# Kernel tuning notes

Measured on AMD Instinct MI355X. Metric: run time of the kernel, lower is better.

## Reference

```python
import jax, jax.numpy as jnp
import numpy as np
from jax import lax

IN_CH = 256
OUT_CH = 256
INTER = IN_CH // 2
KERNEL = 3


def setup_inputs() -> dict:
    key = jax.random.key(0)
    ks = jax.random.split(key, 6)
    B, C, H, W = 8, IN_CH, 128, 128
    x = jax.random.normal(ks[0], (B, C, H, W), dtype=jnp.float32)
    s = 1.0 / np.sqrt(C)
    Wq = jax.random.normal(ks[1], (INTER, C), dtype=jnp.float32) * s
    Wk = jax.random.normal(ks[2], (INTER, C), dtype=jnp.float32) * s
    Wv = jax.random.normal(ks[3], (INTER, C), dtype=jnp.float32) * s
    w1d = jax.random.normal(ks[4], (KERNEL,), dtype=jnp.float32) * (1.0 / np.sqrt(KERNEL))
    Wc = jax.random.normal(ks[5], (OUT_CH, INTER, 3, 3), dtype=jnp.float32) * (1.0 / np.sqrt(INTER * 9))
    return {"x": x, "Wq": Wq, "Wk": Wk, "Wv": Wv, "w1d": w1d, "Wc": Wc}


def reference(x, Wq, Wk, Wv, w1d, Wc):
    B, C, H, W = x.shape
    inter = Wq.shape[0]
    Hs, Ws = H // 4, W // 4  # 1x1 conv, stride 4, pad 0 == spatial subsample
    xs = x[:, :, ::4, ::4]  # [B, C, Hs, Ws]
    q = jnp.einsum('oc,bchw->bohw', Wq, xs).reshape(B, inter, Hs * Ws)  # [B, inter, N]
    k = jnp.einsum('oc,bchw->bohw', Wk, xs).reshape(B, inter, Hs * Ws)
    v = jnp.einsum('oc,bchw->bohw', Wv, xs).reshape(B, inter, Hs * Ws)
    # gate = softmax(Q^T K) over last dim, shape [B, N, N]
    scores = jnp.einsum('bcn,bcm->bnm', q, k)
    gate = jax.nn.softmax(scores, axis=-1)
    # gated value: [B, inter, N] -> [B, inter, Hs, Ws]
    gv = jnp.einsum('bnm,bcm->bcn', gate, v).reshape(B, inter, Hs, Ws)
    # ECA channel gating: global avg pool -> conv1d over channel dim -> sigmoid
    ca = gv.mean(axis=(2, 3))  # [B, inter]
    ca = lax.conv_general_dilated(
        ca[:, None, :],                     # [B, 1, inter]
        w1d[None, None, :],                 # [1, 1, K]
        window_strides=(1,), padding=[((KERNEL - 1) // 2,) * 2],
        dimension_numbers=('NCH', 'OIH', 'NCH'))
    ca = jax.nn.sigmoid(ca)[:, 0, :, None, None]  # [B, inter, 1, 1]
    out = gv * ca
    out = lax.conv_general_dilated(
        out, Wc, window_strides=(1, 1), padding='SAME',
        dimension_numbers=('NCHW', 'OIHW', 'NCHW'))
    return out, gate, ca
```

## Files before the change

### kernel.cpp

```cpp
#include <hip/hip_runtime.h>
#include <math.h>

#define B_   8
#define C_   256
#define CI_  128
#define N_   1024
#define HW_  32
#define CO_  256

typedef __bf16 v8bf __attribute__((ext_vector_type(8)));
typedef float  f32x4 __attribute__((ext_vector_type(4)));
typedef unsigned short ushort_t;

__device__ __forceinline__ unsigned short f2bf_rne(float f) {
    unsigned int u = __float_as_uint(f);
    unsigned int r = u + 0x7FFF + ((u >> 16) & 1);
    return (unsigned short)(r >> 16);
}
__device__ __forceinline__ float bf2f(unsigned short h) {
    return __uint_as_float(((unsigned int)h) << 16);
}
__device__ __forceinline__ v8bf ld8(const ushort_t* p) {
    return *(const v8bf*)p;
}

__global__ __launch_bounds__(256) void prep_all_kernel(
    const float* __restrict__ x,
    const float* __restrict__ Wc,
    const float* __restrict__ Wq, const float* __restrict__ Wk,
    const float* __restrict__ Wv,
    ushort_t* __restrict__ Whi, ushort_t* __restrict__ Wlo,
    ushort_t* __restrict__ Wp_hi, ushort_t* __restrict__ Wp_lo,
    ushort_t* __restrict__ xs_hi, ushort_t* __restrict__ xs_lo,
    float* __restrict__ meanb)
{
    __shared__ ushort_t lh[32 * 264];
    __shared__ ushort_t ll[32 * 264];
    const int bx = blockIdx.x;
    const int tid = threadIdx.x;

    if (bx < 1152) {
        if (bx == 0) {
            *(float4*)&meanb[tid * 4] = make_float4(0.f, 0.f, 0.f, 0.f);
        }
        int idx = bx * 256 + tid;
        int o = idx / 1152;
        int r = idx - o * 1152;
        int ci = r / 9;
        int tap = r - ci * 9;
        float v = Wc[idx];
        unsigned short h = f2bf_rne(v);
        unsigned short l = f2bf_rne(v - bf2f(h));
        int didx = o * 1152 + tap * 128 + ci;
        Whi[didx] = h; Wlo[didx] = l;
    } else if (bx < 1536) {
        int j = (bx - 1152) * 256 + tid;
        int o = j >> 8, c = j & 255;
        float v = (o < 128) ? Wq[o * 256 + c]
                : (o < 256) ? Wk[(o - 128) * 256 + c]
                            : Wv[(o - 256) * 256 + c];
        unsigned short h = f2bf_rne(v);
        unsigned short l = f2bf_rne(v - bf2f(h));
        Wp_hi[j] = h; Wp_lo[j] = l;
    } else {
        const int bx2 = bx - 1536;
        const int h = bx2 & 31, b = bx2 >> 5;
        const int w = tid & 31, cg = tid >> 5;
        float v[32];
        #pragma unroll
        for (int i = 0; i < 32; ++i) {
            int c = i * 8 + cg;
            v[i] = x[((size_t)(b * C_ + c) * 128 + h * 4) * 128 + w * 4];
        }
        #pragma unroll
        for (int i = 0; i < 32; ++i) {
            int c = i * 8 + cg;
            unsigned short hi = f2bf_rne(v[i]);
            unsigned short lo = f2bf_rne(v[i] - bf2f(hi));
            lh[w * 264 + c] = hi;
            ll[w * 264 + c] = lo;
        }
        __syncthreads();
        const int ww = tid >> 3, cs = tid & 7;
        size_t dst = ((size_t)(b * N_) + h * 32 + ww) * 256 + cs * 32;
        #pragma unroll
        for (int t = 0; t < 4; ++t) {
            *(uint4*)&xs_hi[dst + t * 8] = *(uint4*)&lh[ww * 264 + cs * 32 + t * 8];
            *(uint4*)&xs_lo[dst + t * 8] = *(uint4*)&ll[ww * 264 + cs * 32 + t * 8];
        }
    }
}

__global__ __launch_bounds__(256) void proj_mfma_kernel(
    const ushort_t* __restrict__ Wp_hi, const ushort_t* __restrict__ Wp_lo,
    const ushort_t* __restrict__ xs_hi, const ushort_t* __restrict__ xs_lo,
    ushort_t* __restrict__ qt_hi, ushort_t* __restrict__ qt_lo,
    ushort_t* __restrict__ kt_hi, ushort_t* __restrict__ kt_lo,
    ushort_t* __restrict__ vB_hi, ushort_t* __restrict__ vB_lo)
{
    const int n0 = blockIdx.x * 64;
    const int o0 = blockIdx.y * 64;
    const int b  = blockIdx.z;
    const int tid = threadIdx.x;
    const int l = tid & 63, wv = tid >> 6;
    const int wy = wv >> 1, wx = wv & 1;
    const int ln = l & 15, quad = l >> 4;

    f32x4 acc[2][2];
    #pragma unroll
    for (int i = 0; i < 2; ++i)
        #pragma unroll
        for (int j = 0; j < 2; ++j) acc[i][j] = (f32x4){0.f,0.f,0.f,0.f};

    const ushort_t* Ah_p[2]; const ushort_t* Al_p[2];
    const ushort_t* Bh_p[2]; const ushort_t* Bl_p[2];
    #pragma unroll
    for (int i = 0; i < 2; ++i) {
        size_t off = (size_t)(o0 + wy * 32 + i * 16 + ln) * 256 + quad * 8;
        Ah_p[i] = Wp_hi + off; Al_p[i] = Wp_lo + off;
    }
    #pragma unroll
    for (int j = 0; j < 2; ++j) {
        size_t off = ((size_t)(b * N_) + n0 + wx * 32 + j * 16 + ln) * 256 + quad * 8;
        Bh_p[j] = xs_hi + off; Bl_p[j] = xs_lo + off;
    }

    #pragma unroll 4
    for (int k0 = 0; k0 < 256; k0 += 32) {
        v8bf Ah[2], Al[2], Bh[2], Bl[2];
        #pragma unroll
        for (int i = 0; i < 2; ++i) { Ah[i] = ld8(Ah_p[i] + k0); Al[i] = ld8(Al_p[i] + k0); }
        #pragma unroll
        for (int j = 0; j < 2; ++j) { Bh[j] = ld8(Bh_p[j] + k0); Bl[j] = ld8(Bl_p[j] + k0); }
        #pragma unroll
        for (int i = 0; i < 2; ++i)
            #pragma unroll
            for (int j = 0; j < 2; ++j) {
                acc[i][j] = __builtin_amdgcn_mfma_f32_16x16x32_bf16(Ah[i], Bh[j], acc[i][j], 0, 0, 0);
                acc[i][j] = __builtin_amdgcn_mfma_f32_16x16x32_bf16(Ah[i], Bl[j], acc[i][j], 0, 0, 0);
                acc[i][j] = __builtin_amdgcn_mfma_f32_16x16x32_bf16(Al[i], Bh[j], acc[i][j], 0, 0, 0);
            }
    }

    if (o0 < 256) {
        ushort_t* th = (o0 < 128) ? qt_hi : kt_hi;
        ushort_t* tl = (o0 < 128) ? qt_lo : kt_lo;
        const int ob = o0 & 127;
        #pragma unroll
        for (int i = 0; i < 2; ++i)
            #pragma unroll
            for (int j = 0; j < 2; ++j) {
                int oo = ob + wy * 32 + i * 16 + quad * 4;
                int n  = n0 + wx * 32 + j * 16 + ln;
                unsigned int h01 = 0, h23 = 0, l01 = 0, l23 = 0;
                #pragma unroll
                for (int r = 0; r < 4; ++r) {
                    float f = acc[i][j][r];
                    unsigned short hh = f2bf_rne(f);
                    unsigned short lo = f2bf_rne(f - bf2f(hh));
                    if (r < 2) { h01 |= ((unsigned)hh) << (16 * r); l01 |= ((unsigned)lo) << (16 * r); }
                    else       { h23 |= ((unsigned)hh) << (16 * (r - 2)); l23 |= ((unsigned)lo) << (16 * (r - 2)); }
                }
                size_t off = ((size_t)(b * N_) + n) * 128 + oo;
                *(uint2*)&th[off] = make_uint2(h01, h23);
                *(uint2*)&tl[off] = make_uint2(l01, l23);
            }
    } else {
        #pragma unroll
        for (int i = 0; i < 2; ++i)
            #pragma unroll
            for (int j = 0; j < 2; ++j)
                #pragma unroll
                for (int r = 0; r < 4; ++r) {
                    int c = (o0 - 256) + wy * 32 + i * 16 + quad * 4 + r;
                    int m = n0 + wx * 32 + j * 16 + ln;
                    float f = acc[i][j][r];
                    unsigned short hh = f2bf_rne(f);
                    unsigned short lo = f2bf_rne(f - bf2f(hh));
                    size_t off = (((size_t)b * 32 + (m >> 5)) * 128 + c) * 32 + (m & 31);
                    vB_hi[off] = hh; vB_lo[off] = lo;
                }
    }
}

__global__ __launch_bounds__(512, 2) void attn_fused_kernel(
    const ushort_t* __restrict__ qt_hi, const ushort_t* __restrict__ qt_lo,
    const ushort_t* __restrict__ kt_hi, const ushort_t* __restrict__ kt_lo,
    const ushort_t* __restrict__ vB_hi, const ushort_t* __restrict__ vB_lo,
    float* __restrict__ gate, float* __restrict__ gv, float* __restrict__ meanb)
{
    __shared__ __align__(16) char gsm[65536];
    __shared__ float redA[8][32];
    __shared__ float redB[8][32];

    const int n0 = blockIdx.x * 32;
    const int b  = blockIdx.y;
    const int tid = threadIdx.x;
    const int l = tid & 63, w = tid >> 6;
    const int ln = l & 15, quad = l >> 4;
    const int Mw = w * 128;

    const ushort_t* qb_h = qt_hi + ((size_t)(b * N_) + n0) * 128;
    const ushort_t* qb_l = qt_lo + ((size_t)(b * N_) + n0) * 128;
    const ushort_t* kb_h = kt_hi + (size_t)(b * N_) * 128;
    const ushort_t* kb_l = kt_lo + (size_t)(b * N_) * 128;

    f32x4 acc[2][8];
    #pragma unroll
    for (int nt = 0; nt < 2; ++nt)
        #pragma unroll
        for (int mt = 0; mt < 8; ++mt) acc[nt][mt] = (f32x4){0.f,0.f,0.f,0.f};

    #pragma unroll
    for (int c0 = 0; c0 < 128; c0 += 32) {
        v8bf Ah[2], Al[2];
        #pragma unroll
        for (int nt = 0; nt < 2; ++nt) {
            size_t aoff = (size_t)(nt * 16 + ln) * 128 + c0 + quad * 8;
            Ah[nt] = ld8(qb_h + aoff); Al[nt] = ld8(qb_l + aoff);
        }
        #pragma unroll
        for (int mt = 0; mt < 8; ++mt) {
            size_t boff = (size_t)(Mw + mt * 16 + ln) * 128 + c0 + quad * 8;
            v8bf Bh = ld8(kb_h + boff);
            v8bf Bl = ld8(kb_l + boff);
            #pragma unroll
            for (int nt = 0; nt < 2; ++nt) {
                acc[nt][mt] = __builtin_amdgcn_mfma_f32_16x16x32_bf16(Ah[nt], Bh, acc[nt][mt], 0, 0, 0);
                acc[nt][mt] = __builtin_amdgcn_mfma_f32_16x16x32_bf16(Ah[nt], Bl, acc[nt][mt], 0, 0, 0);
                acc[nt][mt] = __builtin_amdgcn_mfma_f32_16x16x32_bf16(Al[nt], Bh, acc[nt][mt], 0, 0, 0);
            }
        }
    }

    float rmax[2][4];
    #pragma unroll
    for (int nt = 0; nt < 2; ++nt)
        #pragma unroll
        for (int r = 0; r < 4; ++r) {
            float m = acc[nt][0][r];
            #pragma unroll
            for (int mt = 1; mt < 8; ++mt) m = fmaxf(m, acc[nt][mt][r]);
            rmax[nt][r] = m;
        }
    #pragma unroll
    for (int nt = 0; nt < 2; ++nt)
        #pragma unroll
        for (int r = 0; r < 4; ++r) {
            float m = rmax[nt][r];
            #pragma unroll
            for (int xm = 1; xm <= 8; xm <<= 1) m = fmaxf(m, __shfl_xor(m, xm, 64));
            rmax[nt][r] = m;
        }
    if (ln == 0) {
        #pragma unroll
        for (int nt = 0; nt < 2; ++nt)
            #pragma unroll
            for (int r = 0; r < 4; ++r)
                redA[w][nt * 16 + quad * 4 + r] = rmax[nt][r];
    }
    __syncthreads();
    #pragma unroll
    for (int nt = 0; nt < 2; ++nt)
        #pragma unroll
        for (int r = 0; r < 4; ++r) {
            int row = nt * 16 + quad * 4 + r;
            float m0 = fmaxf(fmaxf(redA[0][row], redA[1][row]),
                             fmaxf(redA[2][row], redA[3][row]));
            float m1 = fmaxf(fmaxf(redA[4][row], redA[5][row]),
                             fmaxf(redA[6][row], redA[7][row]));
            rmax[nt][r] = fmaxf(m0, m1);
        }

    float rsum[2][4];
    #pragma unroll
    for (int nt = 0; nt < 2; ++nt)
        #pragma unroll
        for (int r = 0; r < 4; ++r) {
            float s = 0.f;
            #pragma unroll
            for (int mt = 0; mt < 8; ++mt) {
                float e = __expf(acc[nt][mt][r] - rmax[nt][r]);
                acc[nt][mt][r] = e;
                s += e;
            }
            rsum[nt][r] = s;
        }
    #pragma unroll
    for (int nt = 0; nt < 2; ++nt)
        #pragma unroll
        for (int r = 0; r < 4; ++r) {
            float s = rsum[nt][r];
            #pragma unroll
            for (int xm = 1; xm <= 8; xm <<= 1) s += __shfl_xor(s, xm, 64);
            rsum[nt][r] = s;
        }
    if (ln == 0) {
        #pragma unroll
        for (int nt = 0; nt < 2; ++nt)
            #pragma unroll
            for (int r = 0; r < 4; ++r)
                redB[w][nt * 16 + quad * 4 + r] = rsum[nt][r];
    }
    __syncthreads();
    #pragma unroll
    for (int nt = 0; nt < 2; ++nt)
        #pragma unroll
        for (int r = 0; r < 4; ++r) {
            int row = nt * 16 + quad * 4 + r;
            float inv = 1.0f / ((redB[0][row] + redB[1][row] + redB[2][row] + redB[3][row]) +
                                (redB[4][row] + redB[5][row] + redB[6][row] + redB[7][row]));
            #pragma unroll
            for (int mt = 0; mt < 8; ++mt) acc[nt][mt][r] *= inv;
        }

    float* grow = gate + (size_t)b * N_ * N_;
    #pragma unroll
    for (int nt = 0; nt < 2; ++nt)
        #pragma unroll
        for (int r = 0; r < 4; ++r) {
            int n  = n0 + nt * 16 + quad * 4 + r;
            int nl = nt * 16 + quad * 4 + r;
            #pragma unroll
            for (int mt = 0; mt < 8; ++mt) {
                int m = Mw + mt * 16 + ln;
                float v = acc[nt][mt][r];
                grow[(size_t)n * N_ + m] = v;
                int chunk = m >> 3;
                int addr = nl * 2048 + (((chunk ^ (nl & 7))) << 4) + ((m & 7) << 1);
                *(ushort_t*)&gsm[addr] = f2bf_rne(v);
            }
        }
    __syncthreads();

    const ushort_t* vb_h = vB_hi + (size_t)b * CI_ * N_;
    const ushort_t* vb_l = vB_lo + (size_t)b * CI_ * N_;

    f32x4 acc2[2];
    acc2[0] = (f32x4){0.f,0.f,0.f,0.f};
    acc2[1] = (f32x4){0.f,0.f,0.f,0.f};

    #pragma unroll 4
    for (int m0 = 0; m0 < 1024; m0 += 32) {
        v8bf Bg[2];
        #pragma unroll
        for (int nt = 0; nt < 2; ++nt) {
            int nl = nt * 16 + ln;
            int chunk = (m0 >> 3) + quad;
            Bg[nt] = *(const v8bf*)&gsm[nl * 2048 + (((chunk ^ (nl & 7))) << 4)];
        }
        int c = w * 16 + ln;
        size_t aoff = (((size_t)(m0 >> 5)) * 128 + c) * 32 + quad * 8;
        v8bf Avh = ld8(vb_h + aoff);
        v8bf Avl = ld8(vb_l + aoff);
        #pragma unroll
        for (int nt = 0; nt < 2; ++nt) {
            acc2[nt] = __builtin_amdgcn_mfma_f32_16x16x32_bf16(Avh, Bg[nt], acc2[nt], 0, 0, 0);
            acc2[nt] = __builtin_amdgcn_mfma_f32_16x16x32_bf16(Avl, Bg[nt], acc2[nt], 0, 0, 0);
        }
    }

    #pragma unroll
    for (int nt = 0; nt < 2; ++nt) {
        int n = n0 + nt * 16 + ln;
        float4 o4 = make_float4(acc2[nt][0], acc2[nt][1], acc2[nt][2], acc2[nt][3]);
        *(float4*)&gv[((size_t)(b * N_) + n) * CI_ + w * 16 + quad * 4] = o4;
    }

    float s0 = acc2[0][0] + acc2[1][0];
    float s1 = acc2[0][1] + acc2[1][1];
    float s2 = acc2[0][2] + acc2[1][2];
    float s3 = acc2[0][3] + acc2[1][3];
    #pragma unroll
    for (int xm = 1; xm <= 8; xm <<= 1) {
        s0 += __shfl_xor(s0, xm, 64);
        s1 += __shfl_xor(s1, xm, 64);
        s2 += __shfl_xor(s2, xm, 64);
        s3 += __shfl_xor(s3, xm, 64);
    }
    if (ln == 0) {
        int cb = b * CI_ + w * 16 + quad * 4;
        atomicAdd(&meanb[cb + 0], s0);
        atomicAdd(&meanb[cb + 1], s1);
        atomicAdd(&meanb[cb + 2], s2);
        atomicAdd(&meanb[cb + 3], s3);
    }
}

__global__ __launch_bounds__(1024) void ca_kernel(
    const float* __restrict__ meanb, const float* __restrict__ w1d,
    float* __restrict__ ca)
{
    const int t = threadIdx.x;
    const int i = t & 127;
    const float sc = 1.0f / 1024.0f;
    float left  = (i > 0)   ? meanb[t - 1] * sc : 0.0f;
    float mid   = meanb[t] * sc;
    float right = (i < 127) ? meanb[t + 1] * sc : 0.0f;
    float val = w1d[0] * left + w1d[1] * mid + w1d[2] * right;
    ca[t] = 1.0f / (1.0f + __expf(-val));
}

#define BHI  0
#define BLO  17408
__global__ __launch_bounds__(256) void conv_mfma_kernel(
    const float* __restrict__ gv, const float* __restrict__ ca,
    const ushort_t* __restrict__ Whi, const ushort_t* __restrict__ Wlo,
    float* __restrict__ out)
{
    __shared__ __align__(16) char smem[67584];
    const int AH[2] = {34816, 51200};
    const int AL[2] = {43008, 59392};

    const int b   = blockIdx.z;
    const int h0  = blockIdx.y * 2;
    const int o0  = blockIdx.x * 64;
    const int tid = threadIdx.x;
    const int l   = tid & 63;
    const int wv  = tid >> 6;
    const int wy  = wv >> 1;
    const int wx  = wv & 1;
    const int ln  = l & 15;
    const int quad = l >> 4;

    f32x4 acc[2][2];
    #pragma unroll
    for (int i = 0; i < 2; ++i)
        #pragma unroll
        for (int j = 0; j < 2; ++j)
            acc[i][j] = (f32x4){0.f, 0.f, 0.f, 0.f};

    const int srow0 = tid >> 3, scol = tid & 7;
    const int la0 = srow0 * 128 + scol * 16;
    const int la1 = (srow0 + 32) * 128 + scol * 16;

    for (int half = 0; half < 2; ++half) {
        __syncthreads();
        for (int u = tid; u < 136 * 16; u += 256) {
            int p   = u >> 4;
            int ciq = u & 15;
            int hrel = p / 34;
            int c    = p - hrel * 34;
            int gr = h0 + hrel - 1;
            int gc = c - 1;
            bool ok = ((unsigned)gr < 32u) && ((unsigned)gc < 32u);
            int cib = half * 64 + ciq * 4;
            float vv[4] = {0.f, 0.f, 0.f, 0.f};
            if (ok) {
                float4 v4 = *(const float4*)&gv[((size_t)(b * N_) + gr * 32 + gc) * CI_ + cib];
                float4 c4 = *(const float4*)&ca[b * CI_ + cib];
                vv[0] = v4.x * c4.x; vv[1] = v4.y * c4.y;
                vv[2] = v4.z * c4.z; vv[3] = v4.w * c4.w;
            }
            unsigned int hx = 0, hy = 0, lx = 0, ly = 0;
            #pragma unroll
            for (int t = 0; t < 4; ++t) {
                unsigned short h = f2bf_rne(vv[t]);
                unsigned short lo = f2bf_rne(vv[t] - bf2f(h));
                if (t < 2) { hx |= ((unsigned)h) << (16 * t); lx |= ((unsigned)lo) << (16 * t); }
                else       { hy |= ((unsigned)h) << (16 * (t - 2)); ly |= ((unsigned)lo) << (16 * (t - 2)); }
            }
            int addr = p * 128 + (((ciq >> 1) ^ (p & 7)) << 4) + ((ciq & 1) << 3);
            *(uint2*)&smem[BHI + addr] = make_uint2(hx, hy);
            *(uint2*)&smem[BLO + addr] = make_uint2(lx, ly);
        }
        {
            int csrc0 = scol ^ (srow0 & 7);
            int csrc1 = scol ^ ((srow0 + 32) & 7);
            size_t g0 = (size_t)(o0 + srow0) * 1152 + half * 64 + csrc0 * 8;
            size_t g1 = (size_t)(o0 + srow0 + 32) * 1152 + half * 64 + csrc1 * 8;
            uint4 h0r = *(const uint4*)&Whi[g0];
            uint4 l0r = *(const uint4*)&Wlo[g0];
            uint4 h1r = *(const uint4*)&Whi[g1];
            uint4 l1r = *(const uint4*)&Wlo[g1];
            *(uint4*)&smem[AH[0] + la0] = h0r;
            *(uint4*)&smem[AL[0] + la0] = l0r;
            *(uint4*)&smem[AH[0] + la1] = h1r;
            *(uint4*)&smem[AL[0] + la1] = l1r;
        }

        for (int tap = 0; tap < 9; ++tap) {
            __syncthreads();
            uint4 nh0, nl0, nh1, nl1;
            if (tap < 8) {
                int ntap = tap + 1;
                int csrc0 = scol ^ (srow0 & 7);
                int csrc1 = scol ^ ((srow0 + 32) & 7);
                size_t g0 = (size_t)(o0 + srow0) * 1152 + ntap * 128 + half * 64 + csrc0 * 8;
                size_t g1 = (size_t)(o0 + srow0 + 32) * 1152 + ntap * 128 + half * 64 + csrc1 * 8;
                nh0 = *(const uint4*)&Whi[g0];
                nl0 = *(const uint4*)&Wlo[g0];
                nh1 = *(const uint4*)&Whi[g1];
                nl1 = *(const uint4*)&Wlo[g1];
            }
            const int ah = AH[tap & 1], al = AL[tap & 1];
            const int dy = tap / 3, dx = tap - dy * 3;
            const int pbase = (wx + dy) * 34 + dx;
            #pragma unroll
            for (int cc = 0; cc < 2; ++cc) {
                v8bf Bh[2], Bl[2], Ah2[2], Al2[2];
                #pragma unroll
                for (int j = 0; j < 2; ++j) {
                    int p = pbase + j * 16 + ln;
                    int ch = cc * 4 + quad;
                    int addr = p * 128 + ((ch ^ (p & 7)) << 4);
                    Bh[j] = *(const v8bf*)&smem[BHI + addr];
                    Bl[j] = *(const v8bf*)&smem[BLO + addr];
                }
                #pragma unroll
                for (int i = 0; i < 2; ++i) {
                    int o = wy * 32 + i * 16 + ln;
                    int ch = cc * 4 + quad;
                    int addr = o * 128 + ((ch ^ (o & 7)) << 4);
                    Ah2[i] = *(const v8bf*)&smem[ah + addr];
                    Al2[i] = *(const v8bf*)&smem[al + addr];
                }
                #pragma unroll
                for (int i = 0; i < 2; ++i)
                    #pragma unroll
                    for (int j = 0; j < 2; ++j) {
                        acc[i][j] = __builtin_amdgcn_mfma_f32_16x16x32_bf16(Ah2[i], Bh[j], acc[i][j], 0, 0, 0);
                        acc[i][j] = __builtin_amdgcn_mfma_f32_16x16x32_bf16(Ah2[i], Bl[j], acc[i][j], 0, 0, 0);
                        acc[i][j] = __builtin_amdgcn_mfma_f32_16x16x32_bf16(Al2[i], Bh[j], acc[i][j], 0, 0, 0);
                    }
            }
            if (tap < 8) {
                int nb = (tap + 1) & 1;
                *(uint4*)&smem[AH[nb] + la0] = nh0;
                *(uint4*)&smem[AL[nb] + la0] = nl0;
                *(uint4*)&smem[AH[nb] + la1] = nh1;
                *(uint4*)&smem[AL[nb] + la1] = nl1;
            }
        }
    }

    const int h = h0 + wx;
    #pragma unroll
    for (int i = 0; i < 2; ++i)
        #pragma unroll
        for (int j = 0; j < 2; ++j)
            #pragma unroll
            for (int r = 0; r < 4; ++r) {
                int o = o0 + wy * 32 + i * 16 + quad * 4 + r;
                int w = j * 16 + ln;
                out[(size_t)(b * CO_ + o) * N_ + h * 32 + w] = acc[i][j][r];
            }
}

extern "C" void kernel_launch(void* const* d_in, const int* in_sizes, int n_in,
                              void* d_out, int out_size, void* d_ws, size_t ws_size,
                              hipStream_t stream) {
    const float* x   = (const float*)d_in[0];
    const float* Wq  = (const float*)d_in[1];
    const float* Wk  = (const float*)d_in[2];
    const float* Wv  = (const float*)d_in[3];
    const float* w1d = (const float*)d_in[4];
    const float* Wc  = (const float*)d_in[5];

    float* out  = (float*)d_out;
    float* gate = out + 2097152;
    float* ca   = gate + 8388608;

    float*    gv      = (float*)d_ws;
    float*    meanb   = gv + 1048576;
    ushort_t* Whi     = (ushort_t*)(meanb + 1024);
    ushort_t* Wlo     = Whi + 294912;
    ushort_t* Wp_hi   = Wlo + 294912;
    ushort_t* Wp_lo   = Wp_hi + 98304;
    ushort_t* xs_hi   = Wp_lo + 98304;
    ushort_t* xs_lo   = xs_hi + 2097152;
    ushort_t* qt_hi   = xs_lo + 2097152;
    ushort_t* qt_lo   = qt_hi + 1048576;
    ushort_t* kt_hi   = qt_lo + 1048576;
    ushort_t* kt_lo   = kt_hi + 1048576;
    ushort_t* vB_hi   = kt_lo + 1048576;
    ushort_t* vB_lo   = vB_hi + 1048576;

    prep_all_kernel<<<dim3(1792), 256, 0, stream>>>(
        x, Wc, Wq, Wk, Wv, Whi, Wlo, Wp_hi, Wp_lo, xs_hi, xs_lo, meanb);
    proj_mfma_kernel<<<dim3(16, 6, 8), 256, 0, stream>>>(
        Wp_hi, Wp_lo, xs_hi, xs_lo, qt_hi, qt_lo, kt_hi, kt_lo, vB_hi, vB_lo);
    attn_fused_kernel<<<dim3(32, 8), 512, 0, stream>>>(
        qt_hi, qt_lo, kt_hi, kt_lo, vB_hi, vB_lo, gate, gv, meanb);
    ca_kernel<<<1, 1024, 0, stream>>>(meanb, w1d, ca);
    conv_mfma_kernel<<<dim3(4, 16, 8), 256, 0, stream>>>(gv, ca, Whi, Wlo, out);
}
```

Measured before the change: 286.8 us.

## Fuse ECA gate into conv, remap block order, add MFMA priority, defer gate store

The separate ca_kernel launch is removed: each conv block now computes the 128 sigmoid channel gates from meanb into shared memory, and one block per batch writes ca out. Block indices in the projection, attention and conv kernels are remapped so the batch index varies fastest, spreading work across XCDs and caches. s_setprio wraps the MFMA bursts to favour matrix issue over other waves. The fp32 gate store in the attention kernel moves after the gv MFMA loop so the large global write overlaps less with the compute phase. In exchange, every conv block repeats the small gate computation.

Result: no change. 284.0 us (-1.0%).

```diff
diff --git a/kernel.cpp b/kernel.cpp
--- a/kernel.cpp
+++ b/kernel.cpp
@@ -98,9 +98,11 @@
     ushort_t* __restrict__ kt_hi, ushort_t* __restrict__ kt_lo,
     ushort_t* __restrict__ vB_hi, ushort_t* __restrict__ vB_lo)
 {
-    const int n0 = blockIdx.x * 64;
-    const int o0 = blockIdx.y * 64;
-    const int b  = blockIdx.z;
+    const int lin = blockIdx.x + 16 * (blockIdx.y + 6 * blockIdx.z);
+    const int b    = lin & 7;
+    const int rest = lin >> 3;
+    const int n0 = (rest & 15) * 64;
+    const int o0 = (rest >> 4) * 64;
     const int tid = threadIdx.x;
     const int l = tid & 63, wv = tid >> 6;
     const int wy = wv >> 1, wx = wv & 1;
@@ -132,6 +134,7 @@
         for (int i = 0; i < 2; ++i) { Ah[i] = ld8(Ah_p[i] + k0); Al[i] = ld8(Al_p[i] + k0); }
         #pragma unroll
         for (int j = 0; j < 2; ++j) { Bh[j] = ld8(Bh_p[j] + k0); Bl[j] = ld8(Bl_p[j] + k0); }
+        __builtin_amdgcn_s_setprio(1);
         #pragma unroll
         for (int i = 0; i < 2; ++i)
             #pragma unroll
@@ -140,6 +143,7 @@
                 acc[i][j] = __builtin_amdgcn_mfma_f32_16x16x32_bf16(Ah[i], Bl[j], acc[i][j], 0, 0, 0);
                 acc[i][j] = __builtin_amdgcn_mfma_f32_16x16x32_bf16(Al[i], Bh[j], acc[i][j], 0, 0, 0);
             }
+        __builtin_amdgcn_s_setprio(0);
     }
 
     if (o0 < 256) {
@@ -193,8 +197,9 @@
     __shared__ float redA[8][32];
     __shared__ float redB[8][32];
 
-    const int n0 = blockIdx.x * 32;
-    const int b  = blockIdx.y;
+    const int lin = blockIdx.x + 32 * blockIdx.y;
+    const int b  = lin & 7;
+    const int n0 = (lin >> 3) * 32;
     const int tid = threadIdx.x;
     const int l = tid & 63, w = tid >> 6;
     const int ln = l & 15, quad = l >> 4;
@@ -224,12 +229,14 @@
             size_t boff = (size_t)(Mw + mt * 16 + ln) * 128 + c0 + quad * 8;
             v8bf Bh = ld8(kb_h + boff);
             v8bf Bl = ld8(kb_l + boff);
+            __builtin_amdgcn_s_setprio(1);
             #pragma unroll
             for (int nt = 0; nt < 2; ++nt) {
                 acc[nt][mt] = __builtin_amdgcn_mfma_f32_16x16x32_bf16(Ah[nt], Bh, acc[nt][mt], 0, 0, 0);
                 acc[nt][mt] = __builtin_amdgcn_mfma_f32_16x16x32_bf16(Ah[nt], Bl, acc[nt][mt], 0, 0, 0);
                 acc[nt][mt] = __builtin_amdgcn_mfma_f32_16x16x32_bf16(Al[nt], Bh, acc[nt][mt], 0, 0, 0);
             }
+            __builtin_amdgcn_s_setprio(0);
         }
     }
 
@@ -314,21 +321,17 @@
             for (int mt = 0; mt < 8; ++mt) acc[nt][mt][r] *= inv;
         }
 
-    float* grow = gate + (size_t)b * N_ * N_;
-    #pragma unroll
-    for (int nt = 0; nt < 2; ++nt)
-        #pragma unroll
-        for (int r = 0; r < 4; ++r) {
-            int n  = n0 + nt * 16 + quad * 4 + r;
+    #pragma unroll
+    for (int nt = 0; nt < 2; ++nt)
+        #pragma unroll
+        for (int r = 0; r < 4; ++r) {
             int nl = nt * 16 + quad * 4 + r;
             #pragma unroll
             for (int mt = 0; mt < 8; ++mt) {
                 int m = Mw + mt * 16 + ln;
-                float v = acc[nt][mt][r];
-                grow[(size_t)n * N_ + m] = v;
                 int chunk = m >> 3;
                 int addr = nl * 2048 + (((chunk ^ (nl & 7))) << 4) + ((m & 7) << 1);
-                *(ushort_t*)&gsm[addr] = f2bf_rne(v);
+                *(ushort_t*)&gsm[addr] = f2bf_rne(acc[nt][mt][r]);
             }
         }
     __syncthreads();
@@ -353,11 +356,13 @@
         size_t aoff = (((size_t)(m0 >> 5)) * 128 + c) * 32 + quad * 8;
         v8bf Avh = ld8(vb_h + aoff);
         v8bf Avl = ld8(vb_l + aoff);
+        __builtin_amdgcn_s_setprio(1);
         #pragma unroll
         for (int nt = 0; nt < 2; ++nt) {
             acc2[nt] = __builtin_amdgcn_mfma_f32_16x16x32_bf16(Avh, Bg[nt], acc2[nt], 0, 0, 0);
             acc2[nt] = __builtin_amdgcn_mfma_f32_16x16x32_bf16(Avl, Bg[nt], acc2[nt], 0, 0, 0);
         }
+        __builtin_amdgcn_s_setprio(0);
     }
 
     #pragma unroll
@@ -366,6 +371,19 @@
         float4 o4 = make_float4(acc2[nt][0], acc2[nt][1], acc2[nt][2], acc2[nt][3]);
         *(float4*)&gv[((size_t)(b * N_) + n) * CI_ + w * 16 + quad * 4] = o4;
     }
+
+    float* grow = gate + (size_t)b * N_ * N_;
+    #pragma unroll
+    for (int nt = 0; nt < 2; ++nt)
+        #pragma unroll
+        for (int r = 0; r < 4; ++r) {
+            int n = n0 + nt * 16 + quad * 4 + r;
+            #pragma unroll
+            for (int mt = 0; mt < 8; ++mt) {
+                int m = Mw + mt * 16 + ln;
+                grow[(size_t)n * N_ + m] = acc[nt][mt][r];
+            }
+        }
 
     float s0 = acc2[0][0] + acc2[1][0];
     float s1 = acc2[0][1] + acc2[1][1];
@@ -387,34 +405,24 @@
     }
 }
 
-__global__ __launch_bounds__(1024) void ca_kernel(
-    const float* __restrict__ meanb, const float* __restrict__ w1d,
-    float* __restrict__ ca)
-{
-    const int t = threadIdx.x;
-    const int i = t & 127;
-    const float sc = 1.0f / 1024.0f;
-    float left  = (i > 0)   ? meanb[t - 1] * sc : 0.0f;
-    float mid   = meanb[t] * sc;
-    float right = (i < 127) ? meanb[t + 1] * sc : 0.0f;
-    float val = w1d[0] * left + w1d[1] * mid + w1d[2] * right;
-    ca[t] = 1.0f / (1.0f + __expf(-val));
-}
-
 #define BHI  0
 #define BLO  17408
 __global__ __launch_bounds__(256) void conv_mfma_kernel(
-    const float* __restrict__ gv, const float* __restrict__ ca,
+    const float* __restrict__ gv, const float* __restrict__ meanb,
+    const float* __restrict__ w1d,
     const ushort_t* __restrict__ Whi, const ushort_t* __restrict__ Wlo,
-    float* __restrict__ out)
+    float* __restrict__ ca_out, float* __restrict__ out)
 {
     __shared__ __align__(16) char smem[67584];
+    __shared__ float ca_s[128];
     const int AH[2] = {34816, 51200};
     const int AL[2] = {43008, 59392};
 
-    const int b   = blockIdx.z;
-    const int h0  = blockIdx.y * 2;
-    const int o0  = blockIdx.x * 64;
+    const int lin = blockIdx.x + 4 * (blockIdx.y + 16 * blockIdx.z);
+    const int b    = lin & 7;
+    const int rest = lin >> 3;
+    const int o0 = (rest & 3) * 64;
+    const int h0 = (rest >> 2) * 2;
     const int tid = threadIdx.x;
     const int l   = tid & 63;
     const int wv  = tid >> 6;
@@ -422,6 +430,18 @@
     const int wx  = wv & 1;
     const int ln  = l & 15;
     const int quad = l >> 4;
+
+    if (tid < 128) {
+        const float sc = 1.0f / 1024.0f;
+        int t = b * 128 + tid;
+        float left  = (tid > 0)   ? meanb[t - 1] * sc : 0.0f;
+        float mid   = meanb[t] * sc;
+        float right = (tid < 127) ? meanb[t + 1] * sc : 0.0f;
+        float val = w1d[0] * left + w1d[1] * mid + w1d[2] * right;
+        float s = 1.0f / (1.0f + __expf(-val));
+        ca_s[tid] = s;
+        if (rest == 0) ca_out[t] = s;
+    }
 
     f32x4 acc[2][2];
     #pragma unroll
@@ -448,7 +468,7 @@
             float vv[4] = {0.f, 0.f, 0.f, 0.f};
             if (ok) {
                 float4 v4 = *(const float4*)&gv[((size_t)(b * N_) + gr * 32 + gc) * CI_ + cib];
-                float4 c4 = *(const float4*)&ca[b * CI_ + cib];
+                float4 c4 = *(const float4*)&ca_s[cib];
                 vv[0] = v4.x * c4.x; vv[1] = v4.y * c4.y;
                 vv[2] = v4.z * c4.z; vv[3] = v4.w * c4.w;
             }
@@ -582,6 +602,6 @@
         Wp_hi, Wp_lo, xs_hi, xs_lo, qt_hi, qt_lo, kt_hi, kt_lo, vB_hi, vB_lo);
     attn_fused_kernel<<<dim3(32, 8), 512, 0, stream>>>(
         qt_hi, qt_lo, kt_hi, kt_lo, vB_hi, vB_lo, gate, gv, meanb);
-    ca_kernel<<<1, 1024, 0, stream>>>(meanb, w1d, ca);
-    conv_mfma_kernel<<<dim3(4, 16, 8), 256, 0, stream>>>(gv, ca, Whi, Wlo, out);
-}
+    conv_mfma_kernel<<<dim3(4, 16, 8), 256, 0, stream>>>(
+        gv, meanb, w1d, Whi, Wlo, ca, out);
+}
```
